# Performance work log

Hardware: AMD Instinct MI355X
Metric: run time of the kernel (lower is better)

The kernel has to match this reference:

```python
import jax, jax.numpy as jnp
import numpy as np

N, D, H1, H2, C, K = 8192, 512, 1024, 512, 10, 64
EPS_BN = 1e-5  # torch BatchNorm1d default eps


def _bn(x, g, b):
    # BatchNorm1d in training mode: per-batch stats, biased variance
    mu = x.mean(axis=0)
    var = x.var(axis=0)
    return (x - mu) / jnp.sqrt(var + EPS_BN) * g + b


def _features(x, ibn_g, ibn_b, W1, b1, g1, bb1, W2, b2, g2, bb2):
    x = _bn(x, ibn_g, ibn_b)                    # input_norm
    h = _bn(jnp.tanh(x @ W1.T + b1), g1, bb1)   # layer 1: Linear -> Tanh -> BN
    h = _bn(jnp.tanh(h @ W2.T + b2), g2, bb2)   # layer 2
    return h                                    # [N, H2]


def _nona_self(fx, fn, y_ohe):
    # sim = -cdist(fx, fn); self-neighbor path (x == x_n): -inf diag + top-k mask
    sq_x = jnp.sum(fx * fx, axis=1)
    sq_n = jnp.sum(fn * fn, axis=1)
    d2 = jnp.maximum(sq_x[:, None] + sq_n[None, :] - 2.0 * (fx @ fn.T), 0.0)
    safe = d2 > 1e-9
    dist = jnp.where(safe, jnp.sqrt(jnp.where(safe, d2, 1.0)), 0.0)
    sim = -dist
    eye = jnp.eye(N, dtype=bool)
    sim = jnp.where(eye, -jnp.inf, sim)         # sim -= inf * I
    _, idx = jax.lax.top_k(sim, K)              # [N, K]
    keep = jnp.zeros((N, N), dtype=bool).at[jnp.arange(N)[:, None], idx].set(True)
    sim = jnp.where(keep, sim, -jnp.inf)        # KNNMask: non-topk -> -inf
    probs = jax.nn.softmax(sim, axis=1)
    return jnp.clip(probs @ y_ohe, 0.0, 1.0)


def setup_inputs() -> dict:
    key = jax.random.key(0)
    ks = jax.random.split(key, 6)
    x = jax.random.normal(ks[0], (N, D), dtype=jnp.float32)
    x_n = x + 0.0  # NONA self-neighbor mode requires x_n == x elementwise
    y_n = jax.random.randint(ks[1], (N,), 0, C, dtype=jnp.int32)
    s1 = 1.0 / np.sqrt(D)
    s2 = 1.0 / np.sqrt(H1)
    W1 = jax.random.uniform(ks[2], (H1, D), jnp.float32, -s1, s1)
    b1 = jax.random.uniform(ks[3], (H1,), jnp.float32, -s1, s1)
    W2 = jax.random.uniform(ks[4], (H2, H1), jnp.float32, -s2, s2)
    b2 = jax.random.uniform(ks[5], (H2,), jnp.float32, -s2, s2)
    return {
        "x": x, "x_n": x_n, "y_n": y_n,
        "ibn_g": jnp.ones((D,), jnp.float32), "ibn_b": jnp.zeros((D,), jnp.float32),
        "W1": W1, "b1": b1, "g1": jnp.ones((H1,), jnp.float32), "bb1": jnp.zeros((H1,), jnp.float32),
        "W2": W2, "b2": b2, "g2": jnp.ones((H2,), jnp.float32), "bb2": jnp.zeros((H2,), jnp.float32),
    }


def reference(x, x_n, y_n, ibn_g, ibn_b, W1, b1, g1, bb1, W2, b2, g2, bb2):
    fx = _features(x, ibn_g, ibn_b, W1, b1, g1, bb1, W2, b2, g2, bb2)
    fn = _features(x_n, ibn_g, ibn_b, W1, b1, g1, bb1, W2, b2, g2, bb2)
    y_ohe = jax.nn.one_hot(y_n, C, dtype=jnp.float32)
    return _nona_self(fx, fn, y_ohe)
```

## Files before the change

### kernel.cpp

```cpp
#include <hip/hip_runtime.h>
#include <math.h>

#define NROWS 8192
#define DIM   512
#define HID1  1024
#define HID2  512
#define NCLS  10
#define KTOP  64
#define KPACK 1024
#define KFULL 1536
#define EPSBAND 0.02f

typedef __attribute__((ext_vector_type(8))) short short8;
typedef __attribute__((ext_vector_type(4))) float f32x4;
typedef __attribute__((ext_vector_type(4))) double f64x4;

__device__ __forceinline__ unsigned short f2bf(float x) {
    unsigned u = __float_as_uint(x);
    u += 0x7FFFu + ((u >> 16) & 1u);
    return (unsigned short)(u >> 16);
}
__device__ __forceinline__ float bf2f(unsigned short h) {
    return __uint_as_float(((unsigned)h) << 16);
}

template <typename T>
__global__ __launch_bounds__(256) void col_stats_partial(
    const T* __restrict__ A, int F, int rowsPerBlock,
    double* __restrict__ pSum, double* __restrict__ pSqs)
{
    int c  = blockIdx.x * 256 + threadIdx.x;
    int r0 = blockIdx.y * rowsPerBlock;
    double s = 0.0, s2 = 0.0;
    for (int r = r0; r < r0 + rowsPerBlock; ++r) {
        double v = (double)A[(size_t)r * F + c];
        s  += v;
        s2 += v * v;
    }
    pSum[(size_t)blockIdx.y * F + c] = s;
    pSqs[(size_t)blockIdx.y * F + c] = s2;
}

__global__ __launch_bounds__(256) void col_stats_final(
    const double* __restrict__ pSum, const double* __restrict__ pSqs,
    const float* __restrict__ g, const float* __restrict__ b,
    double* __restrict__ scale, double* __restrict__ shift, int F, int nPart)
{
    int c = blockIdx.x * 256 + threadIdx.x;
    double s = 0.0, s2 = 0.0;
    for (int p = 0; p < nPart; ++p) {
        s  += pSum[(size_t)p * F + c];
        s2 += pSqs[(size_t)p * F + c];
    }
    double mean = s * (1.0 / NROWS);
    double var  = s2 * (1.0 / NROWS) - mean * mean;
    double sc   = (double)g[c] / sqrt(var + 1e-5);
    scale[c] = sc;
    shift[c] = (double)b[c] - mean * sc;
}

template <typename T>
__global__ __launch_bounds__(256) void gemm_mfma_tanh(
    const T* __restrict__ A, const double* __restrict__ scl, const double* __restrict__ sft,
    const float* __restrict__ W, const float* __restrict__ bias,
    double* __restrict__ out, int Kd, int F)
{
    __shared__ double aS[32 * 67];
    __shared__ double bS[32 * 67];
    const int t = threadIdx.x;
    const int lane = t & 63;
    const int wv = t >> 6;
    const int nwg = gridDim.x;
    const int q = nwg >> 3;
    const int bid = blockIdx.x;
    const int wgid = (bid & 7) * q + (bid >> 3);
    const int fBlocks = F >> 6;
    const int mb = wgid / fBlocks;
    const int fb = wgid - mb * fBlocks;
    const int fBase = fb * 64;
    const int mBase = mb * 64;
    const int srow = t >> 2;
    const int skq  = (t & 3) * 8;

    f64x4 acc[4];
    #pragma unroll
    for (int n = 0; n < 4; ++n) acc[n] = (f64x4){0.0, 0.0, 0.0, 0.0};

    T      areg[8];
    float  wreg[8];
    double sclr[8], sftr[8];

    auto stage_load = [&](int ch) {
        const int kb = ch << 5;
        const T* ap = &A[(size_t)(mBase + srow) * Kd + kb + skq];
        if constexpr (sizeof(T) == 4) {
            float4 x0 = *(const float4*)ap;
            float4 x1 = *(const float4*)(ap + 4);
            areg[0] = x0.x; areg[1] = x0.y; areg[2] = x0.z; areg[3] = x0.w;
            areg[4] = x1.x; areg[5] = x1.y; areg[6] = x1.z; areg[7] = x1.w;
        } else {
            const double2* dp = (const double2*)ap;
            double2 d0 = dp[0], d1 = dp[1], d2 = dp[2], d3 = dp[3];
            areg[0] = d0.x; areg[1] = d0.y; areg[2] = d1.x; areg[3] = d1.y;
            areg[4] = d2.x; areg[5] = d2.y; areg[6] = d3.x; areg[7] = d3.y;
        }
        const float4* wp = (const float4*)&W[(size_t)(fBase + srow) * Kd + kb + skq];
        float4 w0 = wp[0], w1 = wp[1];
        wreg[0] = w0.x; wreg[1] = w0.y; wreg[2] = w0.z; wreg[3] = w0.w;
        wreg[4] = w1.x; wreg[5] = w1.y; wreg[6] = w1.z; wreg[7] = w1.w;
        const double2* sp = (const double2*)&scl[kb + skq];
        const double2* hp = (const double2*)&sft[kb + skq];
        #pragma unroll
        for (int i = 0; i < 4; ++i) {
            double2 sv = sp[i], hv = hp[i];
            sclr[2 * i] = sv.x; sclr[2 * i + 1] = sv.y;
            sftr[2 * i] = hv.x; sftr[2 * i + 1] = hv.y;
        }
    };
    auto stage_write = [&]() {
        #pragma unroll
        for (int i = 0; i < 8; ++i) {
            aS[(skq + i) * 67 + srow] = (double)areg[i] * sclr[i] + sftr[i];
            bS[(skq + i) * 67 + srow] = (double)wreg[i];
        }
    };
    auto compute = [&]() {
        #pragma unroll
        for (int k4 = 0; k4 < 8; ++k4) {
            const int kk = k4 * 4 + (lane >> 4);
            double a = aS[kk * 67 + wv * 16 + (lane & 15)];
            #pragma unroll
            for (int n = 0; n < 4; ++n) {
                double b = bS[kk * 67 + n * 16 + (lane & 15)];
                acc[n] = __builtin_amdgcn_mfma_f64_16x16x4f64(a, b, acc[n], 0, 0, 0);
            }
        }
    };

    const int nChunks = Kd >> 5;
    stage_load(0);
    stage_write();
    __syncthreads();
    for (int ch = 0; ch < nChunks; ++ch) {
        const bool hn = (ch + 1 < nChunks);
        if (hn) stage_load(ch + 1);
        compute();
        __syncthreads();
        if (hn) {
            stage_write();
            __syncthreads();
        }
    }

    #pragma unroll
    for (int n = 0; n < 4; ++n) {
        const int f = fBase + n * 16 + (lane & 15);
        const double bz = (double)bias[f];
        #pragma unroll
        for (int r = 0; r < 4; ++r) {
            const int m = mBase + wv * 16 + (lane >> 4) * 4 + r;
            out[(size_t)m * F + f] = tanh(acc[n][r] + bz);
        }
    }
}

__global__ __launch_bounds__(256) void pack_features(
    const double* __restrict__ y2, const double* __restrict__ scl, const double* __restrict__ sft,
    unsigned short* __restrict__ R, float* __restrict__ sqf)
{
    __shared__ double red[4];
    const int r = blockIdx.x;
    const int t = threadIdx.x;
    const int wid = t >> 6, lane = t & 63;
    const int c = t * 2;
    double2 y  = *(const double2*)&y2[(size_t)r * HID2 + c];
    double2 s2 = *(const double2*)&scl[c];
    double2 h2 = *(const double2*)&sft[c];
    double f0 = y.x * s2.x + h2.x;
    double f1 = y.y * s2.y + h2.y;
    unsigned short hi0 = f2bf((float)f0);
    unsigned short hi1 = f2bf((float)f1);
    unsigned short lo0 = f2bf((float)(f0 - (double)bf2f(hi0)));
    unsigned short lo1 = f2bf((float)(f1 - (double)bf2f(hi1)));
    unsigned short* Rr = R + (size_t)r * KPACK;
    Rr[c]           = hi0; Rr[c + 1]           = hi1;
    Rr[HID2 + c]    = lo0; Rr[HID2 + c + 1]    = lo1;
    double s = f0 * f0 + f1 * f1;
    #pragma unroll
    for (int off = 32; off > 0; off >>= 1) s += __shfl_down(s, off);
    if (lane == 0) red[wid] = s;
    __syncthreads();
    if (t == 0) sqf[r] = (float)(red[0] + red[1] + red[2] + red[3]);
}

__global__ __launch_bounds__(256) void sim_mfma(
    const unsigned short* __restrict__ R, const float* __restrict__ sqf,
    float* __restrict__ simbuf, int rowBase)
{
    __shared__ unsigned short aT[2][128 * 64];
    __shared__ unsigned short bT[2][128 * 64];
    const int t = threadIdx.x;
    const int wid = t >> 6, lane = t & 63;
    const int wr = wid >> 1, wc = wid & 1;
    const int bid  = blockIdx.y * 8 + blockIdx.x;
    const int wgid = (bid & 7) * 64 + (bid >> 3);
    const int ib = wgid & 7;
    const int jb = wgid >> 3;
    const int iBase = rowBase + ib * 128;
    const int jBase = jb * 128;
    const int srow = lane >> 3;
    const int skk  = (((lane & 7) ^ srow) * 8);

    f32x4 zero = {0.f, 0.f, 0.f, 0.f};
    f32x4 acc[4][4];
    #pragma unroll
    for (int m = 0; m < 4; ++m)
        #pragma unroll
        for (int n = 0; n < 4; ++n) acc[m][n] = zero;

    auto STAGE = [&](int buf, int kt) {
        const int k0 = kt * 64;
        const int aSrc = (k0 < 512)  ? k0 : (k0 - 512);
        const int bSrc = (k0 < 1024) ? k0 : (k0 - 1024);
        #pragma unroll
        for (int c = 0; c < 4; ++c) {
            const int row = c * 32 + wid * 8 + srow;
            const unsigned short* gpA = R + (size_t)(iBase + row) * KPACK + aSrc + skk;
            const unsigned short* gpB = R + (size_t)(jBase + row) * KPACK + bSrc + skk;
            unsigned short* lpA = &aT[buf][(c * 4 + wid) * 512];
            unsigned short* lpB = &bT[buf][(c * 4 + wid) * 512];
            __builtin_amdgcn_global_load_lds((const __attribute__((address_space(1))) void*)gpA,
                (__attribute__((address_space(3))) void*)lpA, 16, 0, 0);
            __builtin_amdgcn_global_load_lds((const __attribute__((address_space(1))) void*)gpB,
                (__attribute__((address_space(3))) void*)lpB, 16, 0, 0);
        }
    };

    STAGE(0, 0);
    __syncthreads();
    int cur = 0;
    const int nKT = KFULL / 64;
    for (int kt = 0; kt < nKT; ++kt) {
        if (kt + 1 < nKT) STAGE(cur ^ 1, kt + 1);
        #pragma unroll
        for (int ks = 0; ks < 2; ++ks) {
            short8 aF[4], bF[4];
            #pragma unroll
            for (int m = 0; m < 4; ++m) {
                int rA = wr * 64 + m * 16 + (lane & 15);
                int ck = ((ks * 4 + (lane >> 4)) ^ (lane & 7)) * 8;
                aF[m] = *(const short8*)&aT[cur][rA * 64 + ck];
            }
            #pragma unroll
            for (int n = 0; n < 4; ++n) {
                int rB = wc * 64 + n * 16 + (lane & 15);
                int ck = ((ks * 4 + (lane >> 4)) ^ (lane & 7)) * 8;
                bF[n] = *(const short8*)&bT[cur][rB * 64 + ck];
            }
            #pragma unroll
            for (int m = 0; m < 4; ++m)
                #pragma unroll
                for (int n = 0; n < 4; ++n)
                    acc[m][n] = __builtin_amdgcn_mfma_f32_16x16x32_bf16(aF[m], bF[n], acc[m][n], 0, 0, 0);
        }
        __syncthreads();
        cur ^= 1;
    }

    #pragma unroll
    for (int m = 0; m < 4; ++m) {
        #pragma unroll
        for (int n = 0; n < 4; ++n) {
            int j = jBase + wc * 64 + n * 16 + (lane & 15);
            float sqj = sqf[j];
            #pragma unroll
            for (int r = 0; r < 4; ++r) {
                int i = iBase + wr * 64 + m * 16 + (lane >> 4) * 4 + r;
                float d2 = sqf[i] + sqj - 2.0f * acc[m][n][r];
                d2 = fmaxf(d2, 0.f);
                float s = (i == j) ? -INFINITY : -d2;
                simbuf[(size_t)(i - rowBase) * NROWS + j] = s;
            }
        }
    }
}

__device__ __forceinline__ unsigned fKey(float v) {
    unsigned b = __float_as_uint(v);
    return (b & 0x80000000u) ? ~b : (b | 0x80000000u);
}
__device__ __forceinline__ float keyToFloat(unsigned k) {
    unsigned b = (k & 0x80000000u) ? (k ^ 0x80000000u) : ~k;
    return __uint_as_float(b);
}

__global__ __launch_bounds__(256) void topk_refine(
    const float* __restrict__ simbuf,
    const double* __restrict__ y2, const double* __restrict__ scl, const double* __restrict__ sft,
    const int* __restrict__ labels, float* __restrict__ out, int rowBase)
{
    __shared__ int      redI[4];
    __shared__ unsigned redU[4];
    __shared__ float    redF[4];
    __shared__ float    cls[NCLS];
    __shared__ int      bandJ[128];
    __shared__ double   bandD2[128];
    __shared__ unsigned char keepB[128];
    __shared__ int      bandCnt;

    const int t = threadIdx.x;
    const int wid = t >> 6, lane = t & 63;
    const int row = blockIdx.x;
    const int gi = rowBase + row;
    const float* srow = simbuf + (size_t)row * NROWS;

    unsigned key[32];
    #pragma unroll
    for (int ii = 0; ii < 32; ++ii) key[ii] = fKey(srow[t + ii * 256]);

    unsigned kmax = 0u;
    #pragma unroll
    for (int ii = 0; ii < 32; ++ii) kmax = max(kmax, key[ii]);
    #pragma unroll
    for (int off = 32; off > 0; off >>= 1) kmax = max(kmax, (unsigned)__shfl_down(kmax, off));
    if (lane == 0) redU[wid] = kmax;
    if (t == 0) bandCnt = 0;
    if (t < NCLS) cls[t] = 0.f;
    __syncthreads();
    kmax = max(max(redU[0], redU[1]), max(redU[2], redU[3]));
    float d2min = fmaxf(-keyToFloat(kmax), 0.f);
    float distMin = (d2min > 1e-9f) ? sqrtf(d2min) : 0.f;
    __syncthreads();

    unsigned lo = 0u, hi = 0xFFFFFFFFu;
    while (lo < hi) {
        unsigned mid = (unsigned)(((unsigned long long)lo + hi + 1ull) >> 1);
        int cnt = 0;
        #pragma unroll
        for (int ii = 0; ii < 32; ++ii) cnt += (key[ii] >= mid) ? 1 : 0;
        #pragma unroll
        for (int off = 32; off > 0; off >>= 1) cnt += __shfl_down(cnt, off);
        if (lane == 0) redI[wid] = cnt;
        __syncthreads();
        int tot = redI[0] + redI[1] + redI[2] + redI[3];
        __syncthreads();
        if (tot >= KTOP) lo = mid; else hi = mid - 1u;
    }
    const float s64 = keyToFloat(lo);
    const unsigned Ku = fKey(s64 + EPSBAND);
    const unsigned Kl = fKey(s64 - EPSBAND);

    int cnt = 0;
    #pragma unroll
    for (int ii = 0; ii < 32; ++ii) cnt += (key[ii] >= Ku) ? 1 : 0;
    #pragma unroll
    for (int off = 32; off > 0; off >>= 1) cnt += __shfl_down(cnt, off);
    if (lane == 0) redI[wid] = cnt;
    __syncthreads();
    const int nSafe = redI[0] + redI[1] + redI[2] + redI[3];
    const int Rslots = KTOP - nSafe;

    #pragma unroll
    for (int ii = 0; ii < 32; ++ii) {
        if (key[ii] >= Kl && key[ii] < Ku) {
            int pos = atomicAdd(&bandCnt, 1);
            if (pos < 128) bandJ[pos] = t + ii * 256;
        }
    }
    __syncthreads();
    const int nb = min(bandCnt, 128);

    for (int c2 = wid; c2 < nb; c2 += 4) {
        int j = bandJ[c2];
        double s = 0.0;
        for (int d = lane; d < HID2; d += 64) {
            double sc = scl[d], sh = sft[d];
            double fi = y2[(size_t)gi * HID2 + d] * sc + sh;
            double fj = y2[(size_t)j  * HID2 + d] * sc + sh;
            double df = fi - fj;
            s += df * df;
        }
        #pragma unroll
        for (int off = 32; off > 0; off >>= 1) s += __shfl_down(s, off);
        if (lane == 0) bandD2[c2] = s;
    }
    __syncthreads();

    for (int c2 = t; c2 < nb; c2 += 256) {
        double d2c = bandD2[c2];
        int jc = bandJ[c2];
        int rank = 0;
        for (int q = 0; q < nb; ++q) {
            double dq = bandD2[q];
            rank += (dq < d2c || (dq == d2c && bandJ[q] < jc)) ? 1 : 0;
        }
        keepB[c2] = (rank < Rslots) ? 1 : 0;
    }
    __syncthreads();

    float S = 0.f;
    #pragma unroll
    for (int ii = 0; ii < 32; ++ii) {
        if (key[ii] >= Ku) {
            float d2 = -keyToFloat(key[ii]);
            float dist = (d2 > 1e-9f) ? sqrtf(d2) : 0.f;
            float w = expf(distMin - dist);
            S += w;
            atomicAdd(&cls[labels[t + ii * 256]], w);
        }
    }
    for (int c2 = t; c2 < nb; c2 += 256) {
        if (keepB[c2]) {
            double dd = bandD2[c2];
            float dist = (dd > 1e-9) ? (float)sqrt(dd) : 0.f;
            float w = expf(distMin - dist);
            S += w;
            atomicAdd(&cls[labels[bandJ[c2]]], w);
        }
    }
    #pragma unroll
    for (int off = 32; off > 0; off >>= 1) S += __shfl_down(S, off);
    if (lane == 0) redF[wid] = S;
    __syncthreads();
    float Stot = redF[0] + redF[1] + redF[2] + redF[3];

    if (t < NCLS) {
        float p = cls[t] / Stot;
        out[(size_t)gi * NCLS + t] = fminf(fmaxf(p, 0.f), 1.f);
    }
}

extern "C" void kernel_launch(void* const* d_in, const int* in_sizes, int n_in,
                              void* d_out, int out_size, void* d_ws, size_t ws_size,
                              hipStream_t stream)
{
    const float* x     = (const float*)d_in[0];
    const int*   y_n   = (const int*)d_in[2];
    const float* ibn_g = (const float*)d_in[3];
    const float* ibn_b = (const float*)d_in[4];
    const float* W1    = (const float*)d_in[5];
    const float* b1    = (const float*)d_in[6];
    const float* g1    = (const float*)d_in[7];
    const float* bb1   = (const float*)d_in[8];
    const float* W2    = (const float*)d_in[9];
    const float* b2    = (const float*)d_in[10];
    const float* g2    = (const float*)d_in[11];
    const float* bb2   = (const float*)d_in[12];
    float* out = (float*)d_out;

    char* ws = (char*)d_ws;
    double*         y1   = (double*)(ws);
    float*          simb = (float*)(ws);
    unsigned short* Rp   = (unsigned short*)(ws + 33554432);
    double*         y2   = (double*)(ws + 67108864);
    double*         pSum = (double*)(ws + 100663296);
    double*         pSqs = (double*)(ws + 101187584);
    double*         prm  = (double*)(ws + 101711872);
    double* scale0 = prm;           double* shift0 = prm + 1024;
    double* scale1 = prm + 2048;    double* shift1 = prm + 3072;
    double* scale2 = prm + 4096;    double* shift2 = prm + 5120;
    float*          sqf  = (float*)(ws + 101761024);

    dim3 blk(256);
    const int RPB = NROWS / 64;

    col_stats_partial<float><<<dim3(DIM / 256, 64), blk, 0, stream>>>(x, DIM, RPB, pSum, pSqs);
    col_stats_final<<<dim3(DIM / 256), blk, 0, stream>>>(pSum, pSqs, ibn_g, ibn_b, scale0, shift0, DIM, 64);
    gemm_mfma_tanh<float><<<dim3((NROWS / 64) * (HID1 / 64)), blk, 0, stream>>>(x, scale0, shift0, W1, b1, y1, DIM, HID1);
    col_stats_partial<double><<<dim3(HID1 / 256, 64), blk, 0, stream>>>(y1, HID1, RPB, pSum, pSqs);
    col_stats_final<<<dim3(HID1 / 256), blk, 0, stream>>>(pSum, pSqs, g1, bb1, scale1, shift1, HID1, 64);
    gemm_mfma_tanh<double><<<dim3((NROWS / 64) * (HID2 / 64)), blk, 0, stream>>>(y1, scale1, shift1, W2, b2, y2, HID1, HID2);
    col_stats_partial<double><<<dim3(HID2 / 256, 64), blk, 0, stream>>>(y2, HID2, RPB, pSum, pSqs);
    col_stats_final<<<dim3(HID2 / 256), blk, 0, stream>>>(pSum, pSqs, g2, bb2, scale2, shift2, HID2, 64);
    pack_features<<<dim3(NROWS), blk, 0, stream>>>(y2, scale2, shift2, Rp, sqf);
    for (int ch = 0; ch < 8; ++ch) {
        int rowBase = ch * 1024;
        sim_mfma<<<dim3(8, 64), blk, 0, stream>>>(Rp, sqf, simb, rowBase);
        topk_refine<<<dim3(1024), blk, 0, stream>>>(simb, y2, scale2, shift2, y_n, out, rowBase);
    }
}
```

Before: 1.221 ms.

## Split BN apply out of GEMMs, enlarge GEMM tiles, vectorize top-k refine

Batch-norm scale/shift moves out of the FP64 GEMM staging into separate elementwise kernels. The MLP GEMM tile grows to 128 rows and the bf16 similarity GEMM tile widens to 128x256 with launch_bounds occupancy 1, so each tile reuses more data. The top-k kernel now loads with float4, starts its binary search from the observed min/max key range, and uses per-iteration atomic counters to drop one barrier per step. In exchange it adds extra full passes over the activations, needs more registers and LDS per block, and leaves fewer blocks in flight.

```diff
diff --git a/kernel.cpp b/kernel.cpp
--- a/kernel.cpp
+++ b/kernel.cpp
@@ -59,13 +59,40 @@
     shift[c] = (double)b[c] - mean * sc;
 }
 
-template <typename T>
+__global__ __launch_bounds__(256) void bn_apply_f32(
+    const float* __restrict__ x, const double* __restrict__ scl, const double* __restrict__ sft,
+    double* __restrict__ out)
+{
+    const int base = (blockIdx.x * 256 + threadIdx.x) * 4;
+    float4 v = *(const float4*)&x[base];
+    const int c = base & (DIM - 1);
+    out[base + 0] = (double)v.x * scl[c + 0] + sft[c + 0];
+    out[base + 1] = (double)v.y * scl[c + 1] + sft[c + 1];
+    out[base + 2] = (double)v.z * scl[c + 2] + sft[c + 2];
+    out[base + 3] = (double)v.w * scl[c + 3] + sft[c + 3];
+}
+
+__global__ __launch_bounds__(256) void bn_apply_f64(
+    double* __restrict__ y, const double* __restrict__ scl, const double* __restrict__ sft,
+    int mask)
+{
+    const int base = (blockIdx.x * 256 + threadIdx.x) * 4;
+    const int c = base & mask;
+    double2 v0 = *(const double2*)&y[base];
+    double2 v1 = *(const double2*)&y[base + 2];
+    v0.x = v0.x * scl[c + 0] + sft[c + 0];
+    v0.y = v0.y * scl[c + 1] + sft[c + 1];
+    v1.x = v1.x * scl[c + 2] + sft[c + 2];
+    v1.y = v1.y * scl[c + 3] + sft[c + 3];
+    *(double2*)&y[base]     = v0;
+    *(double2*)&y[base + 2] = v1;
+}
+
 __global__ __launch_bounds__(256) void gemm_mfma_tanh(
-    const T* __restrict__ A, const double* __restrict__ scl, const double* __restrict__ sft,
-    const float* __restrict__ W, const float* __restrict__ bias,
+    const double* __restrict__ A, const float* __restrict__ W, const float* __restrict__ bias,
     double* __restrict__ out, int Kd, int F)
 {
-    __shared__ double aS[32 * 67];
+    __shared__ double aS[32 * 132];
     __shared__ double bS[32 * 67];
     const int t = threadIdx.x;
     const int lane = t & 63;
@@ -78,61 +105,53 @@
     const int mb = wgid / fBlocks;
     const int fb = wgid - mb * fBlocks;
     const int fBase = fb * 64;
-    const int mBase = mb * 64;
-    const int srow = t >> 2;
-    const int skq  = (t & 3) * 8;
-
-    f64x4 acc[4];
-    #pragma unroll
-    for (int n = 0; n < 4; ++n) acc[n] = (f64x4){0.0, 0.0, 0.0, 0.0};
-
-    T      areg[8];
+    const int mBase = mb * 128;
+    const int arow = t >> 1;
+    const int akq  = (t & 1) * 16;
+    const int wrow = t >> 2;
+    const int wkq  = (t & 3) * 8;
+
+    f64x4 acc[2][4];
+    #pragma unroll
+    for (int p = 0; p < 2; ++p)
+        #pragma unroll
+        for (int n = 0; n < 4; ++n) acc[p][n] = (f64x4){0.0, 0.0, 0.0, 0.0};
+
+    double areg[16];
     float  wreg[8];
-    double sclr[8], sftr[8];
 
     auto stage_load = [&](int ch) {
         const int kb = ch << 5;
-        const T* ap = &A[(size_t)(mBase + srow) * Kd + kb + skq];
-        if constexpr (sizeof(T) == 4) {
-            float4 x0 = *(const float4*)ap;
-            float4 x1 = *(const float4*)(ap + 4);
-            areg[0] = x0.x; areg[1] = x0.y; areg[2] = x0.z; areg[3] = x0.w;
-            areg[4] = x1.x; areg[5] = x1.y; areg[6] = x1.z; areg[7] = x1.w;
-        } else {
-            const double2* dp = (const double2*)ap;
-            double2 d0 = dp[0], d1 = dp[1], d2 = dp[2], d3 = dp[3];
-            areg[0] = d0.x; areg[1] = d0.y; areg[2] = d1.x; areg[3] = d1.y;
-            areg[4] = d2.x; areg[5] = d2.y; areg[6] = d3.x; areg[7] = d3.y;
-        }
-        const float4* wp = (const float4*)&W[(size_t)(fBase + srow) * Kd + kb + skq];
+        const double* ap = &A[(size_t)(mBase + arow) * Kd + kb + akq];
+        #pragma unroll
+        for (int j = 0; j < 8; ++j) {
+            double2 v = *(const double2*)(ap + 2 * j);
+            areg[2 * j] = v.x; areg[2 * j + 1] = v.y;
+        }
+        const float4* wp = (const float4*)&W[(size_t)(fBase + wrow) * Kd + kb + wkq];
         float4 w0 = wp[0], w1 = wp[1];
         wreg[0] = w0.x; wreg[1] = w0.y; wreg[2] = w0.z; wreg[3] = w0.w;
         wreg[4] = w1.x; wreg[5] = w1.y; wreg[6] = w1.z; wreg[7] = w1.w;
-        const double2* sp = (const double2*)&scl[kb + skq];
-        const double2* hp = (const double2*)&sft[kb + skq];
-        #pragma unroll
-        for (int i = 0; i < 4; ++i) {
-            double2 sv = sp[i], hv = hp[i];
-            sclr[2 * i] = sv.x; sclr[2 * i + 1] = sv.y;
-            sftr[2 * i] = hv.x; sftr[2 * i + 1] = hv.y;
-        }
     };
     auto stage_write = [&]() {
         #pragma unroll
-        for (int i = 0; i < 8; ++i) {
-            aS[(skq + i) * 67 + srow] = (double)areg[i] * sclr[i] + sftr[i];
-            bS[(skq + i) * 67 + srow] = (double)wreg[i];
-        }
+        for (int i = 0; i < 16; ++i)
+            aS[(akq + i) * 132 + arow] = areg[i];
+        #pragma unroll
+        for (int i = 0; i < 8; ++i)
+            bS[(wkq + i) * 67 + wrow] = (double)wreg[i];
     };
     auto compute = [&]() {
         #pragma unroll
         for (int k4 = 0; k4 < 8; ++k4) {
             const int kk = k4 * 4 + (lane >> 4);
-            double a = aS[kk * 67 + wv * 16 + (lane & 15)];
+            double a0 = aS[kk * 132 + wv * 16 + (lane & 15)];
+            double a1 = aS[kk * 132 + 64 + wv * 16 + (lane & 15)];
             #pragma unroll
             for (int n = 0; n < 4; ++n) {
                 double b = bS[kk * 67 + n * 16 + (lane & 15)];
-                acc[n] = __builtin_amdgcn_mfma_f64_16x16x4f64(a, b, acc[n], 0, 0, 0);
+                acc[0][n] = __builtin_amdgcn_mfma_f64_16x16x4f64(a0, b, acc[0][n], 0, 0, 0);
+                acc[1][n] = __builtin_amdgcn_mfma_f64_16x16x4f64(a1, b, acc[1][n], 0, 0, 0);
             }
         }
     };
@@ -153,13 +172,16 @@
     }
 
     #pragma unroll
-    for (int n = 0; n < 4; ++n) {
-        const int f = fBase + n * 16 + (lane & 15);
-        const double bz = (double)bias[f];
-        #pragma unroll
-        for (int r = 0; r < 4; ++r) {
-            const int m = mBase + wv * 16 + (lane >> 4) * 4 + r;
-            out[(size_t)m * F + f] = tanh(acc[n][r] + bz);
+    for (int p = 0; p < 2; ++p) {
+        #pragma unroll
+        for (int n = 0; n < 4; ++n) {
+            const int f = fBase + n * 16 + (lane & 15);
+            const double bz = (double)bias[f];
+            #pragma unroll
+            for (int r = 0; r < 4; ++r) {
+                const int m = mBase + p * 64 + wv * 16 + (lane >> 4) * 4 + r;
+                out[(size_t)m * F + f] = tanh(acc[p][n][r] + bz);
+            }
         }
     }
 }
@@ -193,30 +215,29 @@
     if (t == 0) sqf[r] = (float)(red[0] + red[1] + red[2] + red[3]);
 }
 
-__global__ __launch_bounds__(256) void sim_mfma(
+__global__ __launch_bounds__(256, 1) void sim_mfma(
     const unsigned short* __restrict__ R, const float* __restrict__ sqf,
     float* __restrict__ simbuf, int rowBase)
 {
     __shared__ unsigned short aT[2][128 * 64];
-    __shared__ unsigned short bT[2][128 * 64];
+    __shared__ unsigned short bT[2][256 * 64];
     const int t = threadIdx.x;
     const int wid = t >> 6, lane = t & 63;
     const int wr = wid >> 1, wc = wid & 1;
-    const int bid  = blockIdx.y * 8 + blockIdx.x;
-    const int wgid = (bid & 7) * 64 + (bid >> 3);
+    const int bid  = blockIdx.x;
+    const int wgid = (bid & 7) * 32 + (bid >> 3);
     const int ib = wgid & 7;
     const int jb = wgid >> 3;
     const int iBase = rowBase + ib * 128;
-    const int jBase = jb * 128;
+    const int jBase = jb * 256;
     const int srow = lane >> 3;
     const int skk  = (((lane & 7) ^ srow) * 8);
 
-    f32x4 zero = {0.f, 0.f, 0.f, 0.f};
-    f32x4 acc[4][4];
+    f32x4 acc[4][8];
     #pragma unroll
     for (int m = 0; m < 4; ++m)
         #pragma unroll
-        for (int n = 0; n < 4; ++n) acc[m][n] = zero;
+        for (int n = 0; n < 8; ++n) acc[m][n] = (f32x4){0.f, 0.f, 0.f, 0.f};
 
     auto STAGE = [&](int buf, int kt) {
         const int k0 = kt * 64;
@@ -224,15 +245,17 @@
         const int bSrc = (k0 < 1024) ? k0 : (k0 - 1024);
         #pragma unroll
         for (int c = 0; c < 4; ++c) {
-            const int row = c * 32 + wid * 8 + srow;
-            const unsigned short* gpA = R + (size_t)(iBase + row) * KPACK + aSrc + skk;
-            const unsigned short* gpB = R + (size_t)(jBase + row) * KPACK + bSrc + skk;
-            unsigned short* lpA = &aT[buf][(c * 4 + wid) * 512];
-            unsigned short* lpB = &bT[buf][(c * 4 + wid) * 512];
-            __builtin_amdgcn_global_load_lds((const __attribute__((address_space(1))) void*)gpA,
-                (__attribute__((address_space(3))) void*)lpA, 16, 0, 0);
-            __builtin_amdgcn_global_load_lds((const __attribute__((address_space(1))) void*)gpB,
-                (__attribute__((address_space(3))) void*)lpB, 16, 0, 0);
+            const int g = wid * 4 + c;
+            const unsigned short* gp = R + (size_t)(iBase + g * 8 + srow) * KPACK + aSrc + skk;
+            __builtin_amdgcn_global_load_lds((const __attribute__((address_space(1))) void*)gp,
+                (__attribute__((address_space(3))) void*)&aT[buf][g * 512], 16, 0, 0);
+        }
+        #pragma unroll
+        for (int c = 0; c < 8; ++c) {
+            const int g = wid * 8 + c;
+            const unsigned short* gp = R + (size_t)(jBase + g * 8 + srow) * KPACK + bSrc + skk;
+            __builtin_amdgcn_global_load_lds((const __attribute__((address_space(1))) void*)gp,
+                (__attribute__((address_space(3))) void*)&bT[buf][g * 512], 16, 0, 0);
         }
     };
 
@@ -244,23 +267,22 @@
         if (kt + 1 < nKT) STAGE(cur ^ 1, kt + 1);
         #pragma unroll
         for (int ks = 0; ks < 2; ++ks) {
-            short8 aF[4], bF[4];
+            const int ck = ((ks * 4 + (lane >> 4)) ^ (lane & 7)) * 8;
+            short8 aF[4], bF[8];
             #pragma unroll
             for (int m = 0; m < 4; ++m) {
                 int rA = wr * 64 + m * 16 + (lane & 15);
-                int ck = ((ks * 4 + (lane >> 4)) ^ (lane & 7)) * 8;
                 aF[m] = *(const short8*)&aT[cur][rA * 64 + ck];
             }
             #pragma unroll
-            for (int n = 0; n < 4; ++n) {
-                int rB = wc * 64 + n * 16 + (lane & 15);
-                int ck = ((ks * 4 + (lane >> 4)) ^ (lane & 7)) * 8;
+            for (int n = 0; n < 8; ++n) {
+                int rB = wc * 128 + n * 16 + (lane & 15);
                 bF[n] = *(const short8*)&bT[cur][rB * 64 + ck];
             }
             #pragma unroll
             for (int m = 0; m < 4; ++m)
                 #pragma unroll
-                for (int n = 0; n < 4; ++n)
+                for (int n = 0; n < 8; ++n)
                     acc[m][n] = __builtin_amdgcn_mfma_f32_16x16x32_bf16(aF[m], bF[n], acc[m][n], 0, 0, 0);
         }
         __syncthreads();
@@ -270,8 +292,8 @@
     #pragma unroll
     for (int m = 0; m < 4; ++m) {
         #pragma unroll
-        for (int n = 0; n < 4; ++n) {
-            int j = jBase + wc * 64 + n * 16 + (lane & 15);
+        for (int n = 0; n < 8; ++n) {
+            int j = jBase + wc * 128 + n * 16 + (lane & 15);
             float sqj = sqf[j];
             #pragma unroll
             for (int r = 0; r < 4; ++r) {
@@ -299,8 +321,8 @@
     const double* __restrict__ y2, const double* __restrict__ scl, const double* __restrict__ sft,
     const int* __restrict__ labels, float* __restrict__ out, int rowBase)
 {
-    __shared__ int      redI[4];
-    __shared__ unsigned redU[4];
+    __shared__ unsigned redU[4], redL[4];
+    __shared__ int      totArr[36];
     __shared__ float    redF[4];
     __shared__ float    cls[NCLS];
     __shared__ int      bandJ[128];
@@ -316,58 +338,77 @@
 
     unsigned key[32];
     #pragma unroll
-    for (int ii = 0; ii < 32; ++ii) key[ii] = fKey(srow[t + ii * 256]);
-
-    unsigned kmax = 0u;
-    #pragma unroll
-    for (int ii = 0; ii < 32; ++ii) kmax = max(kmax, key[ii]);
-    #pragma unroll
-    for (int off = 32; off > 0; off >>= 1) kmax = max(kmax, (unsigned)__shfl_down(kmax, off));
-    if (lane == 0) redU[wid] = kmax;
+    for (int ii = 0; ii < 8; ++ii) {
+        float4 v = ((const float4*)srow)[t + ii * 256];
+        key[ii * 4 + 0] = fKey(v.x);
+        key[ii * 4 + 1] = fKey(v.y);
+        key[ii * 4 + 2] = fKey(v.z);
+        key[ii * 4 + 3] = fKey(v.w);
+    }
+    const unsigned infKey = fKey(-INFINITY);
+
+    unsigned kmax = 0u, kmin = 0xFFFFFFFFu;
+    #pragma unroll
+    for (int ii = 0; ii < 32; ++ii) {
+        kmax = max(kmax, key[ii]);
+        kmin = min(kmin, (key[ii] == infKey) ? 0xFFFFFFFFu : key[ii]);
+    }
+    #pragma unroll
+    for (int off = 32; off > 0; off >>= 1) {
+        kmax = max(kmax, (unsigned)__shfl_down(kmax, off));
+        kmin = min(kmin, (unsigned)__shfl_down(kmin, off));
+    }
+    if (lane == 0) { redU[wid] = kmax; redL[wid] = kmin; }
     if (t == 0) bandCnt = 0;
     if (t < NCLS) cls[t] = 0.f;
+    if (t < 36) totArr[t] = 0;
     __syncthreads();
     kmax = max(max(redU[0], redU[1]), max(redU[2], redU[3]));
+    kmin = min(min(redL[0], redL[1]), min(redL[2], redL[3]));
     float d2min = fmaxf(-keyToFloat(kmax), 0.f);
     float distMin = (d2min > 1e-9f) ? sqrtf(d2min) : 0.f;
-    __syncthreads();
-
-    unsigned lo = 0u, hi = 0xFFFFFFFFu;
+
+    unsigned lo = kmin, hi = kmax;
+    int it = 0;
     while (lo < hi) {
-        unsigned mid = (unsigned)(((unsigned long long)lo + hi + 1ull) >> 1);
+        unsigned mid = lo + ((hi - lo + 1u) >> 1);
         int cnt = 0;
         #pragma unroll
         for (int ii = 0; ii < 32; ++ii) cnt += (key[ii] >= mid) ? 1 : 0;
         #pragma unroll
         for (int off = 32; off > 0; off >>= 1) cnt += __shfl_down(cnt, off);
-        if (lane == 0) redI[wid] = cnt;
+        if (lane == 0) atomicAdd(&totArr[it], cnt);
         __syncthreads();
-        int tot = redI[0] + redI[1] + redI[2] + redI[3];
-        __syncthreads();
+        int tot = totArr[it];
         if (tot >= KTOP) lo = mid; else hi = mid - 1u;
+        ++it;
     }
     const float s64 = keyToFloat(lo);
     const unsigned Ku = fKey(s64 + EPSBAND);
     const unsigned Kl = fKey(s64 - EPSBAND);
 
-    int cnt = 0;
-    #pragma unroll
-    for (int ii = 0; ii < 32; ++ii) cnt += (key[ii] >= Ku) ? 1 : 0;
-    #pragma unroll
-    for (int off = 32; off > 0; off >>= 1) cnt += __shfl_down(cnt, off);
-    if (lane == 0) redI[wid] = cnt;
-    __syncthreads();
-    const int nSafe = redI[0] + redI[1] + redI[2] + redI[3];
+    {
+        int cnt = 0;
+        #pragma unroll
+        for (int ii = 0; ii < 32; ++ii) cnt += (key[ii] >= Ku) ? 1 : 0;
+        #pragma unroll
+        for (int off = 32; off > 0; off >>= 1) cnt += __shfl_down(cnt, off);
+        if (lane == 0) atomicAdd(&totArr[34], cnt);
+    }
+    #pragma unroll
+    for (int ii = 0; ii < 8; ++ii) {
+        #pragma unroll
+        for (int q2 = 0; q2 < 4; ++q2) {
+            unsigned k = key[ii * 4 + q2];
+            if (k >= Kl && k < Ku) {
+                int pos = atomicAdd(&bandCnt, 1);
+                if (pos < 128) bandJ[pos] = (t + ii * 256) * 4 + q2;
+            }
+        }
+    }
+    __syncthreads();
+    const int nSafe = totArr[34];
     const int Rslots = KTOP - nSafe;
-
-    #pragma unroll
-    for (int ii = 0; ii < 32; ++ii) {
-        if (key[ii] >= Kl && key[ii] < Ku) {
-            int pos = atomicAdd(&bandCnt, 1);
-            if (pos < 128) bandJ[pos] = t + ii * 256;
-        }
-    }
-    __syncthreads();
     const int nb = min(bandCnt, 128);
 
     for (int c2 = wid; c2 < nb; c2 += 4) {
@@ -390,9 +431,9 @@
         double d2c = bandD2[c2];
         int jc = bandJ[c2];
         int rank = 0;
-        for (int q = 0; q < nb; ++q) {
-            double dq = bandD2[q];
-            rank += (dq < d2c || (dq == d2c && bandJ[q] < jc)) ? 1 : 0;
+        for (int q2 = 0; q2 < nb; ++q2) {
+            double dq = bandD2[q2];
+            rank += (dq < d2c || (dq == d2c && bandJ[q2] < jc)) ? 1 : 0;
         }
         keepB[c2] = (rank < Rslots) ? 1 : 0;
     }
@@ -400,13 +441,17 @@
 
     float S = 0.f;
     #pragma unroll
-    for (int ii = 0; ii < 32; ++ii) {
-        if (key[ii] >= Ku) {
-            float d2 = -keyToFloat(key[ii]);
-            float dist = (d2 > 1e-9f) ? sqrtf(d2) : 0.f;
-            float w = expf(distMin - dist);
-            S += w;
-            atomicAdd(&cls[labels[t + ii * 256]], w);
+    for (int ii = 0; ii < 8; ++ii) {
+        #pragma unroll
+        for (int q2 = 0; q2 < 4; ++q2) {
+            unsigned k = key[ii * 4 + q2];
+            if (k >= Ku) {
+                float d2 = -keyToFloat(k);
+                float dist = (d2 > 1e-9f) ? sqrtf(d2) : 0.f;
+                float w = expf(distMin - dist);
+                S += w;
+                atomicAdd(&cls[labels[(t + ii * 256) * 4 + q2]], w);
+            }
         }
     }
     for (int c2 = t; c2 < nb; c2 += 256) {
@@ -453,6 +498,7 @@
     float*          simb = (float*)(ws);
     unsigned short* Rp   = (unsigned short*)(ws + 33554432);
     double*         y2   = (double*)(ws + 67108864);
+    double*         xbn  = y2;
     double*         pSum = (double*)(ws + 100663296);
     double*         pSqs = (double*)(ws + 101187584);
     double*         prm  = (double*)(ws + 101711872);
@@ -466,16 +512,18 @@
 
     col_stats_partial<float><<<dim3(DIM / 256, 64), blk, 0, stream>>>(x, DIM, RPB, pSum, pSqs);
     col_stats_final<<<dim3(DIM / 256), blk, 0, stream>>>(pSum, pSqs, ibn_g, ibn_b, scale0, shift0, DIM, 64);
-    gemm_mfma_tanh<float><<<dim3((NROWS / 64) * (HID1 / 64)), blk, 0, stream>>>(x, scale0, shift0, W1, b1, y1, DIM, HID1);
+    bn_apply_f32<<<dim3(NROWS * DIM / 1024), blk, 0, stream>>>(x, scale0, shift0, xbn);
+    gemm_mfma_tanh<<<dim3((NROWS / 128) * (HID1 / 64)), blk, 0, stream>>>(xbn, W1, b1, y1, DIM, HID1);
     col_stats_partial<double><<<dim3(HID1 / 256, 64), blk, 0, stream>>>(y1, HID1, RPB, pSum, pSqs);
     col_stats_final<<<dim3(HID1 / 256), blk, 0, stream>>>(pSum, pSqs, g1, bb1, scale1, shift1, HID1, 64);
-    gemm_mfma_tanh<double><<<dim3((NROWS / 64) * (HID2 / 64)), blk, 0, stream>>>(y1, scale1, shift1, W2, b2, y2, HID1, HID2);
+    bn_apply_f64<<<dim3(NROWS * HID1 / 1024), blk, 0, stream>>>(y1, scale1, shift1, HID1 - 1);
+    gemm_mfma_tanh<<<dim3((NROWS / 128) * (HID2 / 64)), blk, 0, stream>>>(y1, W2, b2, y2, HID1, HID2);
     col_stats_partial<double><<<dim3(HID2 / 256, 64), blk, 0, stream>>>(y2, HID2, RPB, pSum, pSqs);
     col_stats_final<<<dim3(HID2 / 256), blk, 0, stream>>>(pSum, pSqs, g2, bb2, scale2, shift2, HID2, 64);
     pack_features<<<dim3(NROWS), blk, 0, stream>>>(y2, scale2, shift2, Rp, sqf);
     for (int ch = 0; ch < 8; ++ch) {
         int rowBase = ch * 1024;
-        sim_mfma<<<dim3(8, 64), blk, 0, stream>>>(Rp, sqf, simb, rowBase);
+        sim_mfma<<<dim3(256), blk, 0, stream>>>(Rp, sqf, simb, rowBase);
         topk_refine<<<dim3(1024), blk, 0, stream>>>(simb, y2, scale2, shift2, y_n, out, rowBase);
     }
 }
```

After: 1.302 ms. +6.6%, slower.
